# Optimization experiments

Measured on AMD Instinct MI355X. Metric: run time of the kernel, lower is better.

The kernel has to match this reference:

```python
import jax, jax.numpy as jnp
import numpy as np

NUM_HEADS = 16
D_MODEL = 1024
HEAD_DIM = D_MODEL // NUM_HEADS
SCALE = float(np.sqrt(HEAD_DIM))  # NOTE: original multiplies q by sqrt(head_dim)
EPS = 1e-5


def layernorm(x, g, b):
    # LayerNorm over last dim (head_dim), learnable affine
    mu = jnp.mean(x, axis=-1, keepdims=True)
    var = jnp.mean(jnp.square(x - mu), axis=-1, keepdims=True)
    return (x - mu) * jax.lax.rsqrt(var + EPS) * g + b


def setup_inputs() -> dict:
    key = jax.random.key(0)
    ks = jax.random.split(key, 8)
    B, Nq, Nc = 2, 2048, 2048
    s = 0.02
    return {
        "x_query": jax.random.normal(ks[0], (B, Nq, D_MODEL), jnp.float32),
        "x_context": jax.random.normal(ks[1], (B, Nc, D_MODEL), jnp.float32),
        "Wq": jax.random.normal(ks[2], (D_MODEL, D_MODEL), jnp.float32) * s,
        "Wkv": jax.random.normal(ks[3], (D_MODEL, 2 * D_MODEL), jnp.float32) * s,
        "Wp": jax.random.normal(ks[4], (D_MODEL, D_MODEL), jnp.float32) * s,
        "bp": jnp.zeros((D_MODEL,), jnp.float32),
        "ln_g": jnp.ones((HEAD_DIM,), jnp.float32),
        "ln_b": jnp.zeros((HEAD_DIM,), jnp.float32),
    }


def reference(x_query, x_context, Wq, Wkv, Wp, bp, ln_g, ln_b):
    B, Nq, _ = x_query.shape
    Nc = x_context.shape[1]
    H, D = NUM_HEADS, HEAD_DIM
    # projections
    q = (x_query @ Wq).reshape(B, Nq, H, D).transpose(0, 2, 1, 3)  # b h n d
    kv = (x_context @ Wkv).reshape(B, Nc, 2, H, D)
    k = kv[:, :, 0].transpose(0, 2, 1, 3)  # b h n d
    v = kv[:, :, 1].transpose(0, 2, 1, 3)
    # QK-LayerNorm (shared params)
    q = layernorm(q, ln_g, ln_b)
    k = layernorm(k, ln_g, ln_b)
    # NOTE: faithful to source — q is MULTIPLIED by sqrt(head_dim)
    q = q * SCALE
    attn = jnp.einsum("bhqd,bhkd->bhqk", q, k)
    attn = jax.nn.softmax(attn, axis=-1)
    out = jnp.einsum("bhqk,bhkd->bhqd", attn, v)
    out = out.transpose(0, 2, 1, 3).reshape(B, Nq, H * D)
    return out @ Wp + bp
```

## Files before the change

### kernel.cpp

```cpp
#include <hip/hip_runtime.h>
#include <stdint.h>

#define NUM_HEADS 16
#define HEAD_DIM 64
#define D_MODEL 1024
#define SEQ 2048
#define BATCH 2

typedef unsigned short u16;
typedef _Float16 f16x8 __attribute__((ext_vector_type(8)));
typedef float f32x4 __attribute__((ext_vector_type(4)));

__device__ __forceinline__ u16 f2h(float f) {
    _Float16 h = (_Float16)f;
    return __builtin_bit_cast(u16, h);
}
__device__ __forceinline__ float h2f(u16 h) {
    return (float)__builtin_bit_cast(_Float16, h);
}
__device__ __forceinline__ uint32_t pkrtz(float a, float b) {
    return __builtin_bit_cast(uint32_t, __builtin_amdgcn_cvt_pkrtz(a, b));
}

__device__ __forceinline__ float ex2(float x) {
#if __has_builtin(__builtin_amdgcn_exp2f)
    return __builtin_amdgcn_exp2f(x);
#else
    float r;
    asm("v_exp_f32 %0, %1" : "=v"(r) : "v"(x));
    return r;
#endif
}

__device__ __forceinline__ f16x8 ld8h(const u16* p) {
    return *reinterpret_cast<const f16x8*>(p);
}

__device__ __forceinline__ void gl_lds16(const void* g, void* l) {
    __builtin_amdgcn_global_load_lds(
        (const __attribute__((address_space(1))) void*)g,
        (__attribute__((address_space(3))) void*)l,
        16, 0, 0);
}

template <int CTRL>
__device__ __forceinline__ float dpp_mov(float x) {
    return __builtin_bit_cast(float,
        __builtin_amdgcn_update_dpp(0, __builtin_bit_cast(int, x), CTRL, 0xf, 0xf, true));
}
__device__ __forceinline__ float rowsum16(float x) {
    x += dpp_mov<0x121>(x);
    x += dpp_mov<0x122>(x);
    x += dpp_mov<0x124>(x);
    x += dpp_mov<0x128>(x);
    return x;
}

__global__ __launch_bounds__(256) void k_prep(const float* __restrict__ xq,
                                              const float* __restrict__ xc,
                                              const float* __restrict__ Wq,
                                              const float* __restrict__ Wkv,
                                              const float* __restrict__ Wp,
                                              u16* __restrict__ xq16,
                                              u16* __restrict__ xc16,
                                              u16* __restrict__ WqT16,
                                              u16* __restrict__ WkvT16,
                                              u16* __restrict__ WpT16) {
    __shared__ float tile[32][33];
    const int t = blockIdx.x;
    if (t < 8192) {
        int i = t * 256 + threadIdx.x;
        const float* src; u16* dst; int j;
        if (i < 1048576) { src = xq; dst = xq16; j = i; }
        else             { src = xc; dst = xc16; j = i - 1048576; }
        float4 v = reinterpret_cast<const float4*>(src)[j];
        ushort4 o;
        o.x = f2h(v.x); o.y = f2h(v.y); o.z = f2h(v.z); o.w = f2h(v.w);
        reinterpret_cast<ushort4*>(dst)[j] = o;
        return;
    }
    const float* W; u16* WT; int N, bi;
    if (t < 9216)       { W = Wq;  WT = WqT16;  N = 1024; bi = t - 8192; }
    else if (t < 11264) { W = Wkv; WT = WkvT16; N = 2048; bi = t - 9216; }
    else                { W = Wp;  WT = WpT16;  N = 1024; bi = t - 11264; }
    const int K = 1024;
    const int nb = N / 32;
    const int bn = (bi % nb) * 32, bk = (bi / nb) * 32;
    const int tx = threadIdx.x & 31;
    const int ty = threadIdx.x >> 5;
#pragma unroll
    for (int i = 0; i < 32; i += 8)
        tile[ty + i][tx] = W[(size_t)(bk + ty + i) * N + bn + tx];
    __syncthreads();
#pragma unroll
    for (int i = 0; i < 32; i += 8)
        WT[(size_t)(bn + ty + i) * K + bk + tx] = f2h(tile[tx][ty + i]);
}

__device__ __forceinline__ void gemm_mainloop_f16(const u16* __restrict__ A,
                                                  const u16* __restrict__ Bt,
                                                  u16* As, u16* Bs,
                                                  int tileM, int tileN, int K,
                                                  f32x4 acc[4][4]) {
    const int tid = threadIdx.x;
    const int lane = tid & 63;
    const int wv = tid >> 6;
    const int wm = wv >> 1, wn = wv & 1;
    const int quad = lane >> 4, l15 = lane & 15;

    const int c0 = tid, c1 = tid + 256;
    const u16* Ap0 = A + (size_t)(tileM + (c0 >> 2)) * K + (c0 & 3) * 8;
    const u16* Ap1 = A + (size_t)(tileM + (c1 >> 2)) * K + (c1 & 3) * 8;
    const u16* Bp0 = Bt + (size_t)(tileN + (c0 >> 2)) * K + (c0 & 3) * 8;
    const u16* Bp1 = Bt + (size_t)(tileN + (c1 >> 2)) * K + (c1 & 3) * 8;

    for (int k0 = 0; k0 < K; k0 += 32) {
        __syncthreads();
        gl_lds16(Ap0 + k0, &As[c0 * 8]);
        gl_lds16(Ap1 + k0, &As[c1 * 8]);
        gl_lds16(Bp0 + k0, &Bs[c0 * 8]);
        gl_lds16(Bp1 + k0, &Bs[c1 * 8]);
        __syncthreads();
        f16x8 af[4], bfr[4];
#pragma unroll
        for (int mi = 0; mi < 4; ++mi)
            af[mi] = ld8h(&As[(wm * 64 + mi * 16 + l15) * 32 + quad * 8]);
#pragma unroll
        for (int ni = 0; ni < 4; ++ni)
            bfr[ni] = ld8h(&Bs[(wn * 64 + ni * 16 + l15) * 32 + quad * 8]);
#pragma unroll
        for (int mi = 0; mi < 4; ++mi)
#pragma unroll
            for (int ni = 0; ni < 4; ++ni)
                acc[mi][ni] = __builtin_amdgcn_mfma_f32_16x16x32_f16(
                    af[mi], bfr[ni], acc[mi][ni], 0, 0, 0);
    }
}

#define ACC_INIT()                                                   \
    f32x4 acc[4][4];                                                 \
    _Pragma("unroll") for (int i = 0; i < 4; ++i)                    \
        _Pragma("unroll") for (int j = 0; j < 4; ++j)                \
            acc[i][j] = (f32x4){0.f, 0.f, 0.f, 0.f};

__global__ __launch_bounds__(256, 2) void k_proj_f16(const u16* __restrict__ xq16,
                                                     const u16* __restrict__ xc16,
                                                     const u16* __restrict__ WqT16,
                                                     const u16* __restrict__ WkvT16,
                                                     const float* __restrict__ lng,
                                                     const float* __restrict__ lnb,
                                                     u16* __restrict__ Qh_h,
                                                     u16* __restrict__ Qh_l,
                                                     u16* __restrict__ Kh,
                                                     u16* __restrict__ VT) {
    __shared__ __align__(16) u16 As[128 * 32];
    __shared__ __align__(16) u16 Bs[128 * 32];
    const int bx = blockIdx.x;
    const int tileM = blockIdx.y * 128;
    const int tid = threadIdx.x;
    const int lane = tid & 63;
    const int wv = tid >> 6;
    const int wm = wv >> 1, wn = wv & 1;
    const int quad = lane >> 4, l15 = lane & 15;
    ACC_INIT();

    if (bx < 16) {
        const bool isQ = bx < 8;
        const int tileN = (bx & 7) * 128;
        const u16* Axx = isQ ? xq16 : xc16;
        const u16* Bt  = isQ ? WqT16 : WkvT16;
        const float scl = isQ ? 11.5415603294809528f : 1.0f;

        gemm_mainloop_f16(Axx, Bt, As, Bs, tileM, tileN, D_MODEL, acc);

        float gv[4], bv[4];
#pragma unroll
        for (int ni = 0; ni < 4; ++ni) { gv[ni] = lng[ni * 16 + l15]; bv[ni] = lnb[ni * 16 + l15]; }

#pragma unroll
        for (int mi = 0; mi < 4; ++mi) {
#pragma unroll
            for (int r = 0; r < 4; ++r) {
                float sum = 0.f, sq = 0.f;
#pragma unroll
                for (int ni = 0; ni < 4; ++ni) { float x = acc[mi][ni][r]; sum += x; sq += x * x; }
                sum = rowsum16(sum);
                sq  = rowsum16(sq);
                float mu = sum * (1.f / 64.f);
                float var = sq * (1.f / 64.f) - mu * mu;
                float rs = rsqrtf(var + 1e-5f);
                int m = tileM + wm * 64 + mi * 16 + quad * 4 + r;
                int bb = m >> 11, n = m & (SEQ - 1);
#pragma unroll
                for (int ni = 0; ni < 4; ++ni) {
                    int colg = tileN + wn * 64 + ni * 16 + l15;
                    int h = colg >> 6;
                    float y = ((acc[mi][ni][r] - mu) * rs * gv[ni] + bv[ni]) * scl;
                    size_t idx = (((size_t)bb * NUM_HEADS + h) * SEQ + n) * HEAD_DIM + (colg & 63);
                    u16 yh = f2h(y);
                    if (isQ) {
                        Qh_h[idx] = yh;
                        Qh_l[idx] = f2h(y - h2f(yh));
                    } else {
                        Kh[idx] = yh;
                    }
                }
            }
        }
    } else {
        const int tileN = D_MODEL + (bx - 16) * 128;
        gemm_mainloop_f16(xc16, WkvT16, As, Bs, tileM, tileN, D_MODEL, acc);
#pragma unroll
        for (int mi = 0; mi < 4; ++mi) {
            int m0 = tileM + wm * 64 + mi * 16 + quad * 4;
            int bb = m0 >> 11, n0 = m0 & (SEQ - 1);
#pragma unroll
            for (int ni = 0; ni < 4; ++ni) {
                int colg = tileN + wn * 64 + ni * 16 + l15 - D_MODEL;
                int h = colg >> 6, d = colg & 63;
                ushort4 o;
                o.x = f2h(acc[mi][ni][0]);
                o.y = f2h(acc[mi][ni][1]);
                o.z = f2h(acc[mi][ni][2]);
                o.w = f2h(acc[mi][ni][3]);
                *reinterpret_cast<ushort4*>(
                    &VT[(((size_t)bb * NUM_HEADS + h) * HEAD_DIM + d) * SEQ + n0]) = o;
            }
        }
    }
}

__global__ __launch_bounds__(256, 2) void k_gemm_out(const u16* __restrict__ A,
                                                     const u16* __restrict__ Bt,
                                                     const float* __restrict__ bp,
                                                     float* __restrict__ out) {
    __shared__ __align__(16) u16 As[128 * 32];
    __shared__ __align__(16) u16 Bs[128 * 32];
    const int tileM = blockIdx.y * 128, tileN = blockIdx.x * 128;
    const int tid = threadIdx.x;
    const int lane = tid & 63;
    const int wv = tid >> 6;
    const int wm = wv >> 1, wn = wv & 1;
    const int quad = lane >> 4, l15 = lane & 15;
    ACC_INIT();
    gemm_mainloop_f16(A, Bt, As, Bs, tileM, tileN, D_MODEL, acc);

    float bpv[4];
#pragma unroll
    for (int ni = 0; ni < 4; ++ni) bpv[ni] = bp[tileN + wn * 64 + ni * 16 + l15];
#pragma unroll
    for (int mi = 0; mi < 4; ++mi) {
#pragma unroll
        for (int r = 0; r < 4; ++r) {
            int m = tileM + wm * 64 + mi * 16 + quad * 4 + r;
#pragma unroll
            for (int ni = 0; ni < 4; ++ni) {
                int colg = tileN + wn * 64 + ni * 16 + l15;
                out[(size_t)m * D_MODEL + colg] = acc[mi][ni][r] + bpv[ni];
            }
        }
    }
}

__global__ __launch_bounds__(256) void k_attn(const u16* __restrict__ Qh_h,
                                              const u16* __restrict__ Qh_l,
                                              const u16* __restrict__ Kh,
                                              const u16* __restrict__ VT,
                                              u16* __restrict__ AO) {
    __shared__ __align__(16) u16 Ks[2 * 64 * 64];
    __shared__ __align__(16) u16 Vs[2 * 64 * 64];
    __shared__ __align__(16) u16 Ps[64 * 64];

    const int tid = threadIdx.x;
    const int lane = tid & 63;
    const int wv = tid >> 6;
    const int quad = lane >> 4, l15 = lane & 15;
    const int sw = l15 & 3;
    const int w1 = (l15 >> 2) & 1;
    const int id = blockIdx.x;
    const int bh = (id & 7) | (((id >> 8) & 3) << 3);
    const int qt = (id >> 3) & 31;

    const size_t bh_off = (size_t)bh * SEQ * HEAD_DIM;
    const u16* Vbh = VT + (size_t)bh * HEAD_DIM * SEQ;

    f16x8 qfh[2], qfl[2];
#pragma unroll
    for (int kt = 0; kt < 2; ++kt) {
        size_t off = bh_off + (size_t)(qt * 64 + wv * 16 + l15) * HEAD_DIM + kt * 32 + quad * 8;
        qfh[kt] = ld8h(Qh_h + off);
        qfl[kt] = ld8h(Qh_l + off);
    }

    f16x8 ones;
#pragma unroll
    for (int i = 0; i < 8; ++i) ones[i] = (_Float16)1.0f;

    const int rr = lane >> 3;
    const int ss = lane & 7;
    const int cc = ss ^ rr;
    const int row0 = wv * 16 + rr;
    const u16* k0 = Kh + bh_off + (size_t)row0 * HEAD_DIM + cc * 8;
    const u16* v0 = Vbh + (size_t)row0 * SEQ + cc * 8;
    const int ldsW = (wv * 16) * 64;

    f32x4 acc_o[4];
    f32x4 acc_l = (f32x4){0.f, 0.f, 0.f, 0.f};
    float m_i = -3.0e38f;
#pragma unroll
    for (int ni = 0; ni < 4; ++ni) acc_o[ni] = (f32x4){0.f, 0.f, 0.f, 0.f};

    gl_lds16(k0,                &Ks[ldsW]);
    gl_lds16(k0 + 8 * HEAD_DIM, &Ks[ldsW + 8 * 64]);
    gl_lds16(v0,                &Vs[ldsW]);
    gl_lds16(v0 + 8 * SEQ,      &Vs[ldsW + 8 * 64]);

    const int psRow = (wv * 16 + l15) * 64;
    const int psW = psRow + (quad ^ (w1 << 1)) * 4;

    for (int j = 0; j < SEQ / 64; ++j) {
        __syncthreads();
        if (j + 1 < SEQ / 64) {
            const int nb = (j + 1) & 1;
            const size_t ko = (size_t)(j + 1) * 64 * HEAD_DIM;
            const int vo = (j + 1) * 64;
            gl_lds16(k0 + ko,                &Ks[nb * 4096 + ldsW]);
            gl_lds16(k0 + ko + 8 * HEAD_DIM, &Ks[nb * 4096 + ldsW + 8 * 64]);
            gl_lds16(v0 + vo,                &Vs[nb * 4096 + ldsW]);
            gl_lds16(v0 + vo + 8 * SEQ,      &Vs[nb * 4096 + ldsW + 8 * 64]);
        }
        const int bb = (j & 1) * 4096;

        f32x4 acc_s[4];
#pragma unroll
        for (int ni = 0; ni < 4; ++ni) acc_s[ni] = (f32x4){0.f, 0.f, 0.f, 0.f};
#pragma unroll
        for (int kt = 0; kt < 2; ++kt) {
            f16x8 kf[4];
#pragma unroll
            for (int ni = 0; ni < 4; ++ni) {
                int slot = (kt * 4 + quad) ^ (l15 & 7);
                kf[ni] = ld8h(&Ks[bb + (ni * 16 + l15) * 64 + slot * 8]);
            }
#pragma unroll
            for (int ni = 0; ni < 4; ++ni) {
                acc_s[ni] = __builtin_amdgcn_mfma_f32_16x16x32_f16(
                    kf[ni], qfh[kt], acc_s[ni], 0, 0, 0);
                acc_s[ni] = __builtin_amdgcn_mfma_f32_16x16x32_f16(
                    kf[ni], qfl[kt], acc_s[ni], 0, 0, 0);
            }
        }

        float mn[4];
#pragma unroll
        for (int ni = 0; ni < 4; ++ni)
            mn[ni] = fmaxf(fmaxf(acc_s[ni][0], acc_s[ni][1]),
                           fmaxf(acc_s[ni][2], acc_s[ni][3]));
        float mx = fmaxf(fmaxf(mn[0], mn[1]), fmaxf(mn[2], mn[3]));
        mx = fmaxf(mx, __shfl_xor(mx, 16, 64));
        mx = fmaxf(mx, __shfl_xor(mx, 32, 64));
        float mnew = fmaxf(m_i, mx);
        if (__any(mx > m_i)) {
            float alpha = ex2(m_i - mnew);
#pragma unroll
            for (int ni = 0; ni < 4; ++ni) acc_o[ni] *= alpha;
            acc_l[0] *= alpha;
            m_i = mnew;
        }
#pragma unroll
        for (int ni = 0; ni < 4; ++ni) {
            float p0 = ex2(acc_s[ni][0] - mnew);
            float p1 = ex2(acc_s[ni][1] - mnew);
            float p2 = ex2(acc_s[ni][2] - mnew);
            float p3 = ex2(acc_s[ni][3] - mnew);
            uint2 u;
            u.x = pkrtz(p0, p1);
            u.y = pkrtz(p2, p3);
            *reinterpret_cast<uint2*>(&Ps[psW + ((ni ^ sw) * 16)]) = u;
        }

#pragma unroll
        for (int kt = 0; kt < 2; ++kt) {
            int pchunk = (kt * 2 + (quad >> 1)) ^ sw;
            f16x8 pf = ld8h(&Ps[psRow + pchunk * 16 + (((quad & 1) ^ w1) * 8)]);
            f16x8 vf[4];
#pragma unroll
            for (int ni = 0; ni < 4; ++ni) {
                int slot = (kt * 4 + quad) ^ (l15 & 7);
                vf[ni] = ld8h(&Vs[bb + (ni * 16 + l15) * 64 + slot * 8]);
            }
#pragma unroll
            for (int ni = 0; ni < 4; ++ni)
                acc_o[ni] = __builtin_amdgcn_mfma_f32_16x16x32_f16(
                    vf[ni], pf, acc_o[ni], 0, 0, 0);
            acc_l = __builtin_amdgcn_mfma_f32_16x16x32_f16(
                ones, pf, acc_l, 0, 0, 0);
        }
    }

    const float inv = 1.0f / acc_l[0];
#pragma unroll
    for (int ni = 0; ni < 4; ++ni) {
        uint2 u;
        u.x = pkrtz(acc_o[ni][0] * inv, acc_o[ni][1] * inv);
        u.y = pkrtz(acc_o[ni][2] * inv, acc_o[ni][3] * inv);
        *reinterpret_cast<uint2*>(&Ps[psW + ((ni ^ sw) * 16)]) = u;
    }
    const int b = bh >> 4, h = bh & 15;
    const int qrow = qt * 64 + wv * 16 + l15;
    const int echunk = quad ^ sw;
    uint4 o0 = *reinterpret_cast<const uint4*>(&Ps[psRow + echunk * 16 + w1 * 8]);
    uint4 o1 = *reinterpret_cast<const uint4*>(&Ps[psRow + echunk * 16 + (1 - w1) * 8]);
    size_t outb = ((size_t)(b * SEQ + qrow)) * D_MODEL + h * 64 + quad * 16;
    *reinterpret_cast<uint4*>(&AO[outb])     = o0;
    *reinterpret_cast<uint4*>(&AO[outb + 8]) = o1;
}

extern "C" void kernel_launch(void* const* d_in, const int* in_sizes, int n_in,
                              void* d_out, int out_size, void* d_ws, size_t ws_size,
                              hipStream_t stream) {
    const float* xq  = (const float*)d_in[0];
    const float* xc  = (const float*)d_in[1];
    const float* Wq  = (const float*)d_in[2];
    const float* Wkv = (const float*)d_in[3];
    const float* Wp  = (const float*)d_in[4];
    const float* bp  = (const float*)d_in[5];
    const float* lng = (const float*)d_in[6];
    const float* lnb = (const float*)d_in[7];
    float* out = (float*)d_out;

    char* ws = (char*)d_ws;
    const size_t MB = 1 << 20;
    u16* xq16   = (u16*)(ws + 0 * MB);
    u16* xc16   = (u16*)(ws + 8 * MB);
    u16* WqT16  = (u16*)(ws + 16 * MB);
    u16* WkvT16 = (u16*)(ws + 18 * MB);
    u16* WpT16  = (u16*)(ws + 22 * MB);
    u16* Qh_h   = (u16*)(ws + 24 * MB);
    u16* Qh_l   = (u16*)(ws + 32 * MB);
    u16* Kh     = (u16*)(ws + 40 * MB);
    u16* VT     = (u16*)(ws + 48 * MB);
    u16* AO     = xq16;

    k_prep<<<12288, 256, 0, stream>>>(xq, xc, Wq, Wkv, Wp,
                                      xq16, xc16, WqT16, WkvT16, WpT16);
    k_proj_f16<<<dim3(24, 32), 256, 0, stream>>>(xq16, xc16, WqT16, WkvT16,
                                                 lng, lnb, Qh_h, Qh_l, Kh, VT);
    k_attn<<<1024, 256, 0, stream>>>(Qh_h, Qh_l, Kh, VT, AO);
    k_gemm_out<<<dim3(8, 32), 256, 0, stream>>>(AO, WpT16, bp, out);
}
```

Measured before the change: 245.4 us.

## Load K/V fragments directly from global into registers, drop LDS staging

The attention kernel stops staging K and V tiles in shared memory with global_load_lds and a per-tile __syncthreads. Each wave now reads its MFMA K/V fragments straight from global memory in 32-key steps, with K for the next step software-prefetched into a second register set. Only a small per-wave P buffer stays in LDS, which cuts LDS use and block barriers and may raise occupancy. In exchange each of the four waves reloads the same K/V from global/L2 with no sharing inside the block, and the output conversion switches to round-to-nearest.

```diff
diff --git a/kernel.cpp b/kernel.cpp
--- a/kernel.cpp
+++ b/kernel.cpp
@@ -20,6 +20,9 @@
 }
 __device__ __forceinline__ uint32_t pkrtz(float a, float b) {
     return __builtin_bit_cast(uint32_t, __builtin_amdgcn_cvt_pkrtz(a, b));
+}
+__device__ __forceinline__ uint32_t pkrtn(float a, float b) {
+    return (uint32_t)f2h(a) | ((uint32_t)f2h(b) << 16);
 }
 
 __device__ __forceinline__ float ex2(float x) {
@@ -267,22 +270,17 @@
                                               const u16* __restrict__ Kh,
                                               const u16* __restrict__ VT,
                                               u16* __restrict__ AO) {
-    __shared__ __align__(16) u16 Ks[2 * 64 * 64];
-    __shared__ __align__(16) u16 Vs[2 * 64 * 64];
-    __shared__ __align__(16) u16 Ps[64 * 64];
+    __shared__ __align__(16) u16 Ps[4 * 16 * 32];
 
     const int tid = threadIdx.x;
     const int lane = tid & 63;
     const int wv = tid >> 6;
     const int quad = lane >> 4, l15 = lane & 15;
-    const int sw = l15 & 3;
-    const int w1 = (l15 >> 2) & 1;
     const int id = blockIdx.x;
     const int bh = (id & 7) | (((id >> 8) & 3) << 3);
     const int qt = (id >> 3) & 31;
 
     const size_t bh_off = (size_t)bh * SEQ * HEAD_DIM;
-    const u16* Vbh = VT + (size_t)bh * HEAD_DIM * SEQ;
 
     f16x8 qfh[2], qfl[2];
 #pragma unroll
@@ -296,13 +294,8 @@
 #pragma unroll
     for (int i = 0; i < 8; ++i) ones[i] = (_Float16)1.0f;
 
-    const int rr = lane >> 3;
-    const int ss = lane & 7;
-    const int cc = ss ^ rr;
-    const int row0 = wv * 16 + rr;
-    const u16* k0 = Kh + bh_off + (size_t)row0 * HEAD_DIM + cc * 8;
-    const u16* v0 = Vbh + (size_t)row0 * SEQ + cc * 8;
-    const int ldsW = (wv * 16) * 64;
+    const u16* Kp = Kh + bh_off + (size_t)l15 * HEAD_DIM + quad * 8;
+    const u16* Vp = VT + (size_t)bh * HEAD_DIM * SEQ + (size_t)l15 * SEQ + quad * 8;
 
     f32x4 acc_o[4];
     f32x4 acc_l = (f32x4){0.f, 0.f, 0.f, 0.f};
@@ -310,110 +303,88 @@
 #pragma unroll
     for (int ni = 0; ni < 4; ++ni) acc_o[ni] = (f32x4){0.f, 0.f, 0.f, 0.f};
 
-    gl_lds16(k0,                &Ks[ldsW]);
-    gl_lds16(k0 + 8 * HEAD_DIM, &Ks[ldsW + 8 * 64]);
-    gl_lds16(v0,                &Vs[ldsW]);
-    gl_lds16(v0 + 8 * SEQ,      &Vs[ldsW + 8 * 64]);
-
-    const int psRow = (wv * 16 + l15) * 64;
-    const int psW = psRow + (quad ^ (w1 << 1)) * 4;
-
-    for (int j = 0; j < SEQ / 64; ++j) {
-        __syncthreads();
-        if (j + 1 < SEQ / 64) {
-            const int nb = (j + 1) & 1;
-            const size_t ko = (size_t)(j + 1) * 64 * HEAD_DIM;
-            const int vo = (j + 1) * 64;
-            gl_lds16(k0 + ko,                &Ks[nb * 4096 + ldsW]);
-            gl_lds16(k0 + ko + 8 * HEAD_DIM, &Ks[nb * 4096 + ldsW + 8 * 64]);
-            gl_lds16(v0 + vo,                &Vs[nb * 4096 + ldsW]);
-            gl_lds16(v0 + vo + 8 * SEQ,      &Vs[nb * 4096 + ldsW + 8 * 64]);
-        }
-        const int bb = (j & 1) * 4096;
-
-        f32x4 acc_s[4];
-#pragma unroll
-        for (int ni = 0; ni < 4; ++ni) acc_s[ni] = (f32x4){0.f, 0.f, 0.f, 0.f};
-#pragma unroll
-        for (int kt = 0; kt < 2; ++kt) {
-            f16x8 kf[4];
-#pragma unroll
-            for (int ni = 0; ni < 4; ++ni) {
-                int slot = (kt * 4 + quad) ^ (l15 & 7);
-                kf[ni] = ld8h(&Ks[bb + (ni * 16 + l15) * 64 + slot * 8]);
-            }
-#pragma unroll
-            for (int ni = 0; ni < 4; ++ni) {
-                acc_s[ni] = __builtin_amdgcn_mfma_f32_16x16x32_f16(
-                    kf[ni], qfh[kt], acc_s[ni], 0, 0, 0);
-                acc_s[ni] = __builtin_amdgcn_mfma_f32_16x16x32_f16(
-                    kf[ni], qfl[kt], acc_s[ni], 0, 0, 0);
-            }
-        }
-
-        float mn[4];
-#pragma unroll
-        for (int ni = 0; ni < 4; ++ni)
-            mn[ni] = fmaxf(fmaxf(acc_s[ni][0], acc_s[ni][1]),
-                           fmaxf(acc_s[ni][2], acc_s[ni][3]));
-        float mx = fmaxf(fmaxf(mn[0], mn[1]), fmaxf(mn[2], mn[3]));
-        mx = fmaxf(mx, __shfl_xor(mx, 16, 64));
-        mx = fmaxf(mx, __shfl_xor(mx, 32, 64));
-        float mnew = fmaxf(m_i, mx);
-        if (__any(mx > m_i)) {
-            float alpha = ex2(m_i - mnew);
-#pragma unroll
-            for (int ni = 0; ni < 4; ++ni) acc_o[ni] *= alpha;
-            acc_l[0] *= alpha;
-            m_i = mnew;
-        }
-#pragma unroll
-        for (int ni = 0; ni < 4; ++ni) {
-            float p0 = ex2(acc_s[ni][0] - mnew);
-            float p1 = ex2(acc_s[ni][1] - mnew);
-            float p2 = ex2(acc_s[ni][2] - mnew);
-            float p3 = ex2(acc_s[ni][3] - mnew);
-            uint2 u;
-            u.x = pkrtz(p0, p1);
-            u.y = pkrtz(p2, p3);
-            *reinterpret_cast<uint2*>(&Ps[psW + ((ni ^ sw) * 16)]) = u;
-        }
-
-#pragma unroll
-        for (int kt = 0; kt < 2; ++kt) {
-            int pchunk = (kt * 2 + (quad >> 1)) ^ sw;
-            f16x8 pf = ld8h(&Ps[psRow + pchunk * 16 + (((quad & 1) ^ w1) * 8)]);
-            f16x8 vf[4];
-#pragma unroll
-            for (int ni = 0; ni < 4; ++ni) {
-                int slot = (kt * 4 + quad) ^ (l15 & 7);
-                vf[ni] = ld8h(&Vs[bb + (ni * 16 + l15) * 64 + slot * 8]);
-            }
-#pragma unroll
-            for (int ni = 0; ni < 4; ++ni)
-                acc_o[ni] = __builtin_amdgcn_mfma_f32_16x16x32_f16(
-                    vf[ni], pf, acc_o[ni], 0, 0, 0);
-            acc_l = __builtin_amdgcn_mfma_f32_16x16x32_f16(
-                ones, pf, acc_l, 0, 0, 0);
-        }
+    const int psRow = (wv * 16 + l15) * 32;
+
+#define LDK(dst, J, NI, KT) dst = ld8h(Kp + (size_t)(J) * 2048 + (NI) * 1024 + (KT) * 32)
+#define LDV(dst, J, NI4) dst = ld8h(Vp + (size_t)(NI4) * (16 * SEQ) + (J) * 32)
+#define MFMA16(A, B, C) __builtin_amdgcn_mfma_f32_16x16x32_f16(A, B, C, 0, 0, 0)
+
+#define ATTN_BODY(J, k00, k01, k10, k11, n00, n01, n10, n11)                   \
+    {                                                                          \
+                   \
+        f16x8 vf0, vf1, vf2, vf3;                                              \
+        LDV(vf0, (J), 0); LDV(vf1, (J), 1); LDV(vf2, (J), 2); LDV(vf3, (J), 3);\
+                \
+        f32x4 s0 = (f32x4){0.f, 0.f, 0.f, 0.f};                                \
+        f32x4 s1 = (f32x4){0.f, 0.f, 0.f, 0.f};                                \
+        s0 = MFMA16(k00, qfh[0], s0); s0 = MFMA16(k00, qfl[0], s0);            \
+        s0 = MFMA16(k01, qfh[1], s0); s0 = MFMA16(k01, qfl[1], s0);            \
+        s1 = MFMA16(k10, qfh[0], s1); s1 = MFMA16(k10, qfl[0], s1);            \
+        s1 = MFMA16(k11, qfh[1], s1); s1 = MFMA16(k11, qfl[1], s1);            \
+                   \
+        LDK(n00, (J) + 1, 0, 0); LDK(n01, (J) + 1, 0, 1);                      \
+        LDK(n10, (J) + 1, 1, 0); LDK(n11, (J) + 1, 1, 1);                      \
+            \
+        float mx = fmaxf(fmaxf(fmaxf(s0[0], s0[1]), fmaxf(s0[2], s0[3])),      \
+                         fmaxf(fmaxf(s1[0], s1[1]), fmaxf(s1[2], s1[3])));     \
+        mx = fmaxf(mx, __shfl_xor(mx, 16, 64));                                \
+        mx = fmaxf(mx, __shfl_xor(mx, 32, 64));                                \
+        float mnew = fmaxf(m_i, mx);                                           \
+        if (__any(mx > m_i)) {                \
+            float alpha = ex2(m_i - mnew);                                     \
+            acc_o[0] *= alpha; acc_o[1] *= alpha;                              \
+            acc_o[2] *= alpha; acc_o[3] *= alpha;                              \
+            acc_l[0] *= alpha;                                                 \
+            m_i = mnew;                                                        \
+        }                                                                      \
+        float p0 = ex2(s0[0] - mnew), p1 = ex2(s0[1] - mnew);                  \
+        float p2 = ex2(s0[2] - mnew), p3 = ex2(s0[3] - mnew);                  \
+        float p4 = ex2(s1[0] - mnew), p5 = ex2(s1[1] - mnew);                  \
+        float p6 = ex2(s1[2] - mnew), p7 = ex2(s1[3] - mnew);                  \
+        uint2 ua, ub;                                                          \
+        ua.x = pkrtz(p0, p1); ua.y = pkrtz(p2, p3);                            \
+        ub.x = pkrtz(p4, p5); ub.y = pkrtz(p6, p7);                            \
+        *reinterpret_cast<uint2*>(&Ps[psRow + quad * 4]) = ua;                 \
+        *reinterpret_cast<uint2*>(&Ps[psRow + 16 + quad * 4]) = ub;            \
+            \
+        f16x8 pf = ld8h(&Ps[psRow + quad * 8]);                                \
+                                            \
+        acc_o[0] = MFMA16(vf0, pf, acc_o[0]);                                  \
+        acc_o[1] = MFMA16(vf1, pf, acc_o[1]);                                  \
+        acc_o[2] = MFMA16(vf2, pf, acc_o[2]);                                  \
+        acc_o[3] = MFMA16(vf3, pf, acc_o[3]);                                  \
+        acc_l = MFMA16(ones, pf, acc_l);                                       \
+    }
+
+    f16x8 a00, a01, a10, a11, b00, b01, b10, b11;
+    LDK(a00, 0, 0, 0); LDK(a01, 0, 0, 1); LDK(a10, 0, 1, 0); LDK(a11, 0, 1, 1);
+
+    for (int j = 0; j < SEQ / 32; j += 2) {
+        ATTN_BODY(j,     a00, a01, a10, a11, b00, b01, b10, b11);
+        ATTN_BODY(j + 1, b00, b01, b10, b11, a00, a01, a10, a11);
+        __builtin_amdgcn_s_barrier();
     }
 
     const float inv = 1.0f / acc_l[0];
-#pragma unroll
-    for (int ni = 0; ni < 4; ++ni) {
-        uint2 u;
-        u.x = pkrtz(acc_o[ni][0] * inv, acc_o[ni][1] * inv);
-        u.y = pkrtz(acc_o[ni][2] * inv, acc_o[ni][3] * inv);
-        *reinterpret_cast<uint2*>(&Ps[psW + ((ni ^ sw) * 16)]) = u;
-    }
     const int b = bh >> 4, h = bh & 15;
     const int qrow = qt * 64 + wv * 16 + l15;
-    const int echunk = quad ^ sw;
-    uint4 o0 = *reinterpret_cast<const uint4*>(&Ps[psRow + echunk * 16 + w1 * 8]);
-    uint4 o1 = *reinterpret_cast<const uint4*>(&Ps[psRow + echunk * 16 + (1 - w1) * 8]);
-    size_t outb = ((size_t)(b * SEQ + qrow)) * D_MODEL + h * 64 + quad * 16;
-    *reinterpret_cast<uint4*>(&AO[outb])     = o0;
-    *reinterpret_cast<uint4*>(&AO[outb + 8]) = o1;
+    size_t outb = ((size_t)(b * SEQ + qrow)) * D_MODEL + h * 64 + quad * 8;
+#pragma unroll
+    for (int p = 0; p < 2; ++p) {
+        uint2 u0, u1;
+        u0.x = pkrtn(acc_o[2 * p][0] * inv, acc_o[2 * p][1] * inv);
+        u0.y = pkrtn(acc_o[2 * p][2] * inv, acc_o[2 * p][3] * inv);
+        u1.x = pkrtn(acc_o[2 * p + 1][0] * inv, acc_o[2 * p + 1][1] * inv);
+        u1.y = pkrtn(acc_o[2 * p + 1][2] * inv, acc_o[2 * p + 1][3] * inv);
+        *reinterpret_cast<uint2*>(&Ps[psRow + quad * 4]) = u0;
+        *reinterpret_cast<uint2*>(&Ps[psRow + 16 + quad * 4]) = u1;
+        uint4 ov = *reinterpret_cast<const uint4*>(&Ps[psRow + quad * 8]);
+        *reinterpret_cast<uint4*>(&AO[outb + p * 32]) = ov;
+    }
+#undef LDK
+#undef LDV
+#undef MFMA16
+#undef ATTN_BODY
 }
 
 extern "C" void kernel_launch(void* const* d_in, const int* in_sizes, int n_in,
```

Result: slower. 392.2 us (+59.8%).

## Software-pipeline QK^T one tile ahead of softmax/PV with triple-buffered V

Applied to the files above, without the earlier changes.

Restructures the attention loop so the QK^T MFMAs for tile t+1 are issued before the softmax and PV for tile t. This lets the matrix work overlap the exp/max VALU work, and loads are prefetched two tiles ahead. V gets a third LDS buffer so its lifetime matches the deeper prefetch, which raises LDS use and register pressure from the extra score accumulator. The final output conversion also switches from round-toward-zero to round-to-nearest packing, an accuracy tweak.

```diff
diff --git a/kernel.cpp b/kernel.cpp
--- a/kernel.cpp
+++ b/kernel.cpp
@@ -20,6 +20,9 @@
 }
 __device__ __forceinline__ uint32_t pkrtz(float a, float b) {
     return __builtin_bit_cast(uint32_t, __builtin_amdgcn_cvt_pkrtz(a, b));
+}
+__device__ __forceinline__ uint32_t pkrtn(float a, float b) {
+    return (uint32_t)f2h(a) | ((uint32_t)f2h(b) << 16);
 }
 
 __device__ __forceinline__ float ex2(float x) {
@@ -268,7 +271,7 @@
                                               const u16* __restrict__ VT,
                                               u16* __restrict__ AO) {
     __shared__ __align__(16) u16 Ks[2 * 64 * 64];
-    __shared__ __align__(16) u16 Vs[2 * 64 * 64];
+    __shared__ __align__(16) u16 Vs[3 * 64 * 64];
     __shared__ __align__(16) u16 Ps[64 * 64];
 
     const int tid = threadIdx.x;
@@ -310,52 +313,58 @@
 #pragma unroll
     for (int ni = 0; ni < 4; ++ni) acc_o[ni] = (f32x4){0.f, 0.f, 0.f, 0.f};
 
-    gl_lds16(k0,                &Ks[ldsW]);
-    gl_lds16(k0 + 8 * HEAD_DIM, &Ks[ldsW + 8 * 64]);
-    gl_lds16(v0,                &Vs[ldsW]);
-    gl_lds16(v0 + 8 * SEQ,      &Vs[ldsW + 8 * 64]);
-
     const int psRow = (wv * 16 + l15) * 64;
     const int psW = psRow + (quad ^ (w1 << 1)) * 4;
 
-    for (int j = 0; j < SEQ / 64; ++j) {
+#define MFMA16(A, B, C) __builtin_amdgcn_mfma_f32_16x16x32_f16(A, B, C, 0, 0, 0)
+
+#define STAGE(T, KS, VS)                                                     \
+    do {                                                                     \
+        const size_t ko_ = (size_t)(T) * 64 * HEAD_DIM;                      \
+        const int vo_ = (T) * 64;                                            \
+        gl_lds16(k0 + ko_,                &Ks[(KS) * 4096 + ldsW]);          \
+        gl_lds16(k0 + ko_ + 8 * HEAD_DIM, &Ks[(KS) * 4096 + ldsW + 8 * 64]); \
+        gl_lds16(v0 + vo_,                &Vs[(VS) * 4096 + ldsW]);          \
+        gl_lds16(v0 + vo_ + 8 * SEQ,      &Vs[(VS) * 4096 + ldsW + 8 * 64]); \
+    } while (0)
+
+#define QKCOMP(SREG, KS)                                                     \
+    do {                                                                     \
+        _Pragma("unroll") for (int kt = 0; kt < 2; ++kt) {                   \
+            f16x8 kf[4];                                                     \
+            _Pragma("unroll") for (int ni = 0; ni < 4; ++ni) {               \
+                int slot = (kt * 4 + quad) ^ (l15 & 7);                      \
+                kf[ni] = ld8h(&Ks[(KS) * 4096 + (ni * 16 + l15) * 64 + slot * 8]); \
+            }                                                                \
+            _Pragma("unroll") for (int ni = 0; ni < 4; ++ni) {               \
+                SREG[ni] = MFMA16(kf[ni], qfh[kt], SREG[ni]);                \
+                SREG[ni] = MFMA16(kf[ni], qfl[kt], SREG[ni]);                \
+            }                                                                \
+        }                                                                    \
+    } while (0)
+
+    STAGE(0, 0, 0);
+    __syncthreads();
+    f32x4 s[4];
+#pragma unroll
+    for (int ni = 0; ni < 4; ++ni) s[ni] = (f32x4){0.f, 0.f, 0.f, 0.f};
+    QKCOMP(s, 0);
+    STAGE(1, 1, 1);
+
+    for (int t = 0; t < SEQ / 64; ++t) {
         __syncthreads();
-        if (j + 1 < SEQ / 64) {
-            const int nb = (j + 1) & 1;
-            const size_t ko = (size_t)(j + 1) * 64 * HEAD_DIM;
-            const int vo = (j + 1) * 64;
-            gl_lds16(k0 + ko,                &Ks[nb * 4096 + ldsW]);
-            gl_lds16(k0 + ko + 8 * HEAD_DIM, &Ks[nb * 4096 + ldsW + 8 * 64]);
-            gl_lds16(v0 + vo,                &Vs[nb * 4096 + ldsW]);
-            gl_lds16(v0 + vo + 8 * SEQ,      &Vs[nb * 4096 + ldsW + 8 * 64]);
-        }
-        const int bb = (j & 1) * 4096;
-
-        f32x4 acc_s[4];
-#pragma unroll
-        for (int ni = 0; ni < 4; ++ni) acc_s[ni] = (f32x4){0.f, 0.f, 0.f, 0.f};
-#pragma unroll
-        for (int kt = 0; kt < 2; ++kt) {
-            f16x8 kf[4];
-#pragma unroll
-            for (int ni = 0; ni < 4; ++ni) {
-                int slot = (kt * 4 + quad) ^ (l15 & 7);
-                kf[ni] = ld8h(&Ks[bb + (ni * 16 + l15) * 64 + slot * 8]);
-            }
-#pragma unroll
-            for (int ni = 0; ni < 4; ++ni) {
-                acc_s[ni] = __builtin_amdgcn_mfma_f32_16x16x32_f16(
-                    kf[ni], qfh[kt], acc_s[ni], 0, 0, 0);
-                acc_s[ni] = __builtin_amdgcn_mfma_f32_16x16x32_f16(
-                    kf[ni], qfl[kt], acc_s[ni], 0, 0, 0);
-            }
-        }
+        if (t + 2 < SEQ / 64) STAGE(t + 2, t & 1, (t + 2) % 3);
+
+        f32x4 sn[4];
+#pragma unroll
+        for (int ni = 0; ni < 4; ++ni) sn[ni] = (f32x4){0.f, 0.f, 0.f, 0.f};
+        if (t + 1 < SEQ / 64) QKCOMP(sn, (t + 1) & 1);
 
         float mn[4];
 #pragma unroll
         for (int ni = 0; ni < 4; ++ni)
-            mn[ni] = fmaxf(fmaxf(acc_s[ni][0], acc_s[ni][1]),
-                           fmaxf(acc_s[ni][2], acc_s[ni][3]));
+            mn[ni] = fmaxf(fmaxf(s[ni][0], s[ni][1]),
+                           fmaxf(s[ni][2], s[ni][3]));
         float mx = fmaxf(fmaxf(mn[0], mn[1]), fmaxf(mn[2], mn[3]));
         mx = fmaxf(mx, __shfl_xor(mx, 16, 64));
         mx = fmaxf(mx, __shfl_xor(mx, 32, 64));
@@ -369,16 +378,17 @@
         }
 #pragma unroll
         for (int ni = 0; ni < 4; ++ni) {
-            float p0 = ex2(acc_s[ni][0] - mnew);
-            float p1 = ex2(acc_s[ni][1] - mnew);
-            float p2 = ex2(acc_s[ni][2] - mnew);
-            float p3 = ex2(acc_s[ni][3] - mnew);
+            float p0 = ex2(s[ni][0] - mnew);
+            float p1 = ex2(s[ni][1] - mnew);
+            float p2 = ex2(s[ni][2] - mnew);
+            float p3 = ex2(s[ni][3] - mnew);
             uint2 u;
             u.x = pkrtz(p0, p1);
             u.y = pkrtz(p2, p3);
             *reinterpret_cast<uint2*>(&Ps[psW + ((ni ^ sw) * 16)]) = u;
         }
 
+        const int vb = (t % 3) * 4096;
 #pragma unroll
         for (int kt = 0; kt < 2; ++kt) {
             int pchunk = (kt * 2 + (quad >> 1)) ^ sw;
@@ -387,23 +397,24 @@
 #pragma unroll
             for (int ni = 0; ni < 4; ++ni) {
                 int slot = (kt * 4 + quad) ^ (l15 & 7);
-                vf[ni] = ld8h(&Vs[bb + (ni * 16 + l15) * 64 + slot * 8]);
+                vf[ni] = ld8h(&Vs[vb + (ni * 16 + l15) * 64 + slot * 8]);
             }
 #pragma unroll
             for (int ni = 0; ni < 4; ++ni)
-                acc_o[ni] = __builtin_amdgcn_mfma_f32_16x16x32_f16(
-                    vf[ni], pf, acc_o[ni], 0, 0, 0);
-            acc_l = __builtin_amdgcn_mfma_f32_16x16x32_f16(
-                ones, pf, acc_l, 0, 0, 0);
-        }
+                acc_o[ni] = MFMA16(vf[ni], pf, acc_o[ni]);
+            acc_l = MFMA16(ones, pf, acc_l);
+        }
+
+#pragma unroll
+        for (int ni = 0; ni < 4; ++ni) s[ni] = sn[ni];
     }
 
     const float inv = 1.0f / acc_l[0];
 #pragma unroll
     for (int ni = 0; ni < 4; ++ni) {
         uint2 u;
-        u.x = pkrtz(acc_o[ni][0] * inv, acc_o[ni][1] * inv);
-        u.y = pkrtz(acc_o[ni][2] * inv, acc_o[ni][3] * inv);
+        u.x = pkrtn(acc_o[ni][0] * inv, acc_o[ni][1] * inv);
+        u.y = pkrtn(acc_o[ni][2] * inv, acc_o[ni][3] * inv);
         *reinterpret_cast<uint2*>(&Ps[psW + ((ni ^ sw) * 16)]) = u;
     }
     const int b = bh >> 4, h = bh & 15;
@@ -414,6 +425,9 @@
     size_t outb = ((size_t)(b * SEQ + qrow)) * D_MODEL + h * 64 + quad * 16;
     *reinterpret_cast<uint4*>(&AO[outb])     = o0;
     *reinterpret_cast<uint4*>(&AO[outb + 8]) = o1;
+#undef MFMA16
+#undef STAGE
+#undef QKCOMP
 }
 
 extern "C" void kernel_launch(void* const* d_in, const int* in_sizes, int n_in,
```

New measurement: 245.6 us. No clear change (+0.1%).
